# Optimization experiments

Hardware: AMD Instinct MI355X
Metric: run time of the kernel (lower is better)

Reference implementation:

```python
import jax, jax.numpy as jnp
import numpy as np

HID = 768          # args.hidden_size
LSTM2 = 768        # args.lstm_dim * 2
SCALE = HID ** -0.5


def _cross_attn(q_in, kv_in, Wq, bq, Wk, bk, Wv, bv):
    # Linear projections (weights stored as [in, out])
    Q = q_in @ Wq + bq            # [B, Sq, H]
    K = kv_in @ Wk + bk           # [B, Sk, H]
    V = kv_in @ Wv + bv           # [B, Sk, H]
    attn = jnp.einsum('bqh,bkh->bqk', Q, K) * SCALE
    attn = jax.nn.softmax(attn, axis=-1)
    return jnp.einsum('bqk,bkh->bqh', attn, V)


def setup_inputs() -> dict:
    key = jax.random.key(0)
    ks = jax.random.split(key, 14)
    B, Ssyn, Ssem = 4, 4096, 2048
    syntactic_feat = jax.random.normal(ks[0], (B, Ssyn, LSTM2), jnp.float32)
    semantic_feat = jax.random.normal(ks[1], (B, Ssem, HID), jnp.float32)

    def lin(k, fan_in, fan_out):
        kw, kb = jax.random.split(k)
        bound = 1.0 / np.sqrt(fan_in)
        W = jax.random.uniform(kw, (fan_in, fan_out), jnp.float32, -bound, bound)
        b = jax.random.uniform(kb, (fan_out,), jnp.float32, -bound, bound)
        return W, b

    # syntax_to_semantic: query_dim=HID, key_dim=LSTM2
    Wq1, bq1 = lin(ks[2], HID, HID)
    Wk1, bk1 = lin(ks[3], LSTM2, HID)
    Wv1, bv1 = lin(ks[4], LSTM2, HID)
    # semantic_to_syntax: query_dim=LSTM2, key_dim=HID
    Wq2, bq2 = lin(ks[5], LSTM2, HID)
    Wk2, bk2 = lin(ks[6], HID, HID)
    Wv2, bv2 = lin(ks[7], HID, HID)
    return dict(syntactic_feat=syntactic_feat, semantic_feat=semantic_feat,
                Wq1=Wq1, bq1=bq1, Wk1=Wk1, bk1=bk1, Wv1=Wv1, bv1=bv1,
                Wq2=Wq2, bq2=bq2, Wk2=Wk2, bk2=bk2, Wv2=Wv2, bv2=bv2)


def reference(syntactic_feat, semantic_feat,
              Wq1, bq1, Wk1, bk1, Wv1, bv1,
              Wq2, bq2, Wk2, bk2, Wv2, bv2):
    # enhanced_semantic: queries from semantic, keys/values from syntactic
    enhanced_semantic = _cross_attn(semantic_feat, syntactic_feat,
                                    Wq1, bq1, Wk1, bk1, Wv1, bv1)
    # enhanced_syntax: queries from syntactic, keys/values from semantic
    enhanced_syntax = _cross_attn(syntactic_feat, semantic_feat,
                                  Wq2, bq2, Wk2, bk2, Wv2, bv2)
    return enhanced_semantic, enhanced_syntax
```

## Files before the change

kernel.cpp:

```cpp
#include <hip/hip_runtime.h>
#include <stdint.h>


typedef unsigned short u16;
typedef __attribute__((ext_vector_type(8))) __bf16 bf16x8;
typedef __attribute__((ext_vector_type(4))) float f32x4;

__device__ __forceinline__ float bf2f(u16 u) {
  union { unsigned int i; float f; } x; x.i = ((unsigned int)u) << 16; return x.f;
}
__device__ __forceinline__ u16 f2bf(float f) {
  union { float f; unsigned int i; } x; x.f = f;
  unsigned int i = x.i;
  i += 0x7fffu + ((i >> 16) & 1u);
  return (u16)(i >> 16);
}

__device__ __forceinline__ void cp16(void* lds, const void* g) {
  __builtin_amdgcn_global_load_lds((__attribute__((address_space(1))) void*)g,
                                   (__attribute__((address_space(3))) void*)lds,
                                   16, 0, 0);
}

struct GemmDesc {
  const u16* A; const u16* Bt; const float* bias; void* C;
  long sA, sB, sC;
  int K, lda, ldb, ldc;
  int gx, gy;
  int start;
  int mode, outf;
  float scale;
};
struct GemmPack { GemmDesc d[6]; int nd; };

__global__ __launch_bounds__(256)
void gemm_multi_kernel(GemmPack p)
{
  __shared__ __align__(16) u16 Asl[128 * 32];
  __shared__ __align__(16) u16 Bsl[128 * 32];

  int seg = 0;
#pragma unroll
  for (int t = 1; t < 6; ++t)
    if (t < p.nd && (int)blockIdx.x >= p.d[t].start) seg = t;
  const GemmDesc& g = p.d[seg];
  const int local = (int)blockIdx.x - g.start;
  const int pxy = g.gx * g.gy;
  const int bz = local / pxy;
  const int rem = local - bz * pxy;
  const int by = rem / g.gx;
  const int bx = rem - by * g.gx;

  const int tid  = threadIdx.x;
  const int lane = tid & 63;
  const int wave = tid >> 6;
  const int l15  = lane & 15;
  const int quad = lane >> 4;
  const int mw   = (wave >> 1) * 64;
  const int nw   = (wave & 1) * 64;

  const char* Ab = (const char*)(g.A + (long)bz * g.sA + (long)bx * 128 * g.lda);
  const char* Bb = (const char*)(g.Bt + (long)bz * g.sB + (long)by * 128 * g.ldb);

  const int o   = wave * 1024 + lane * 16;
  const int mst = o >> 6;
  const int cl  = (o >> 4) & 3;
  const int sst = (mst + (mst >> 2)) & 3;
  const int off = (cl ^ sst) << 4;
  char* ldsA = (char*)Asl + wave * 1024;
  char* ldsB = (char*)Bsl + wave * 1024;
  const long ldaB = (long)g.lda * 2;
  const long ldbB = (long)g.ldb * 2;
  const char* pa0 = Ab + (long)mst * ldaB + off;
  const char* pb0 = Bb + (long)mst * ldbB + off;

  int ia[4], ib[4];
#pragma unroll
  for (int i = 0; i < 4; ++i) {
    const int m = mw + i * 16 + l15;
    ia[i] = m * 4 + (quad ^ ((m + (m >> 2)) & 3));
    const int n = nw + i * 16 + l15;
    ib[i] = n * 4 + (quad ^ ((n + (n >> 2)) & 3));
  }

  f32x4 acc[4][4];
  {
    f32x4 zz = {0.f, 0.f, 0.f, 0.f};
#pragma unroll
    for (int i = 0; i < 4; ++i)
#pragma unroll
      for (int j = 0; j < 4; ++j) acc[i][j] = zz;
  }

  const int nk = g.K >> 5;
  for (int kk = 0; kk < nk; ++kk) {
    const long kb = (long)kk << 6;
    cp16(ldsA,        pa0 + kb);
    cp16(ldsA + 4096, pa0 + kb + 64 * ldaB);
    cp16(ldsB,        pb0 + kb);
    cp16(ldsB + 4096, pb0 + kb + 64 * ldbB);
    __syncthreads();

    bf16x8 a[4], b[4];
    const bf16x8* As8 = (const bf16x8*)Asl;
    const bf16x8* Bs8 = (const bf16x8*)Bsl;
#pragma unroll
    for (int i = 0; i < 4; ++i) a[i] = As8[ia[i]];
#pragma unroll
    for (int j = 0; j < 4; ++j) b[j] = Bs8[ib[j]];
#pragma unroll
    for (int i = 0; i < 4; ++i)
#pragma unroll
      for (int j = 0; j < 4; ++j)
        acc[i][j] = __builtin_amdgcn_mfma_f32_16x16x32_bf16(a[i], b[j], acc[i][j], 0, 0, 0);
    __syncthreads();
  }

  const int brow = bx * 128 + mw + quad * 4;
  const int bcol = by * 128 + nw + l15;
  float cb[4];
  if (g.mode == 1) {
#pragma unroll
    for (int j = 0; j < 4; ++j) cb[j] = g.bias[bcol + j * 16];
  }
#pragma unroll
  for (int i = 0; i < 4; ++i) {
    const int r0 = brow + i * 16;
    float rb[4];
    if (g.mode == 2) {
#pragma unroll
      for (int r = 0; r < 4; ++r) rb[r] = g.bias[r0 + r];
    }
#pragma unroll
    for (int j = 0; j < 4; ++j) {
      const int col = bcol + j * 16;
#pragma unroll
      for (int r = 0; r < 4; ++r) {
        float x = acc[i][j][r] * g.scale;
        if (g.mode == 1) x += cb[j];
        if (g.mode == 2) x += rb[r];
        const long idx = (long)bz * g.sC + (long)(r0 + r) * g.ldc + col;
        if (g.outf) ((float*)g.C)[idx] = x;
        else        ((u16*)g.C)[idx] = f2bf(x);
      }
    }
  }
}

__global__ __launch_bounds__(256)
void cvt2_bf16_kernel(const float* __restrict__ sa, u16* __restrict__ da, int n8a,
                      const float* __restrict__ sb, u16* __restrict__ db, int n8b)
{
  int idx = blockIdx.x * 256 + threadIdx.x;
  const float* src; u16* dst; int i;
  if (idx < n8a) { src = sa; dst = da; i = idx; }
  else           { src = sb; dst = db; i = idx - n8a; if (i >= n8b) return; }
  const float4* s4 = (const float4*)src;
  float4 a = s4[i * 2], b = s4[i * 2 + 1];
  uint4 o;
  o.x = (unsigned int)f2bf(a.x) | ((unsigned int)f2bf(a.y) << 16);
  o.y = (unsigned int)f2bf(a.z) | ((unsigned int)f2bf(a.w) << 16);
  o.z = (unsigned int)f2bf(b.x) | ((unsigned int)f2bf(b.y) << 16);
  o.w = (unsigned int)f2bf(b.z) | ((unsigned int)f2bf(b.w) << 16);
  ((uint4*)dst)[i] = o;
}

__global__ void transpose6_kernel(const float* s0, const float* s1, const float* s2,
                                  const float* s3, const float* s4, const float* s5,
                                  u16* d0, u16* d1, u16* d2,
                                  u16* d3, u16* d4, u16* d5)
{
  __shared__ float t[32][33];
  const float* src; u16* dst;
  switch (blockIdx.z) {
    case 0: src = s0; dst = d0; break;
    case 1: src = s1; dst = d1; break;
    case 2: src = s2; dst = d2; break;
    case 3: src = s3; dst = d3; break;
    case 4: src = s4; dst = d4; break;
    default: src = s5; dst = d5; break;
  }
  const int tx = threadIdx.x, ty = threadIdx.y;
  const int x = blockIdx.x * 32 + tx;
  const int y0 = blockIdx.y * 32;
#pragma unroll
  for (int j = 0; j < 32; j += 8) t[ty + j][tx] = src[(long)(y0 + ty + j) * 768 + x];
  __syncthreads();
  const int x2 = y0 + tx;
#pragma unroll
  for (int j = 0; j < 32; j += 8)
    dst[(long)(blockIdx.x * 32 + ty + j) * 768 + x2] = f2bf(t[tx][ty + j]);
}

template <int NV>
__device__ __forceinline__ void softmax_row(u16* row)
{
  __shared__ float red[8];
  const int tid  = threadIdx.x;
  const int lane = tid & 63;
  const int wave = tid >> 6;
  uint4* p4 = (uint4*)row;

  uint4 ld[NV / 8];
#pragma unroll
  for (int c = 0; c < NV / 8; ++c) ld[c] = p4[tid + c * 256];
  float v[NV];
#pragma unroll
  for (int c = 0; c < NV / 8; ++c) {
    unsigned int w[4] = {ld[c].x, ld[c].y, ld[c].z, ld[c].w};
#pragma unroll
    for (int q = 0; q < 4; ++q) {
      v[c * 8 + q * 2]     = bf2f((u16)(w[q] & 0xffffu));
      v[c * 8 + q * 2 + 1] = bf2f((u16)(w[q] >> 16));
    }
  }

  float m = -1e30f;
#pragma unroll
  for (int i = 0; i < NV; ++i) m = fmaxf(m, v[i]);
#pragma unroll
  for (int off = 32; off > 0; off >>= 1) m = fmaxf(m, __shfl_xor(m, off, 64));
  if (lane == 0) red[wave] = m;
  __syncthreads();
  m = fmaxf(fmaxf(red[0], red[1]), fmaxf(red[2], red[3]));

  float s = 0.f;
#pragma unroll
  for (int i = 0; i < NV; ++i) { v[i] = __expf(v[i] - m); s += v[i]; }
#pragma unroll
  for (int off = 32; off > 0; off >>= 1) s += __shfl_xor(s, off, 64);
  if (lane == 0) red[4 + wave] = s;
  __syncthreads();
  s = (red[4] + red[5]) + (red[6] + red[7]);
  const float inv = 1.0f / s;

#pragma unroll
  for (int c = 0; c < NV / 8; ++c) {
    unsigned int w[4];
#pragma unroll
    for (int q = 0; q < 4; ++q) {
      const u16 lo = f2bf(v[c * 8 + q * 2] * inv);
      const u16 hi = f2bf(v[c * 8 + q * 2 + 1] * inv);
      w[q] = (unsigned int)lo | ((unsigned int)hi << 16);
    }
    uint4 st; st.x = w[0]; st.y = w[1]; st.z = w[2]; st.w = w[3];
    p4[tid + c * 256] = st;
  }
}

__global__ __launch_bounds__(256)
void softmax_both_kernel(u16* S1, u16* S2)
{
  if (blockIdx.x < 8192) softmax_row<16>(S1 + (long)blockIdx.x * 4096);
  else                   softmax_row<8>(S2 + (long)(blockIdx.x - 8192) * 2048);
}


static GemmDesc mkdesc(const void* A, const void* Bt, const float* bias, void* C,
                       long sA, long sB, long sC, int K, int lda, int ldb, int ldc,
                       int M, int N, int start, int mode, int outf, float scale)
{
  GemmDesc d;
  d.A = (const u16*)A; d.Bt = (const u16*)Bt; d.bias = bias; d.C = C;
  d.sA = sA; d.sB = sB; d.sC = sC;
  d.K = K; d.lda = lda; d.ldb = ldb; d.ldc = ldc;
  d.gx = M / 128; d.gy = N / 128; d.start = start;
  d.mode = mode; d.outf = outf; d.scale = scale;
  return d;
}

extern "C" void kernel_launch(void* const* d_in, const int* in_sizes, int n_in,
                              void* d_out, int out_size, void* d_ws, size_t ws_size,
                              hipStream_t stream)
{
  (void)in_sizes; (void)n_in; (void)out_size; (void)ws_size;
  const float* syn = (const float*)d_in[0];
  const float* sem = (const float*)d_in[1];
  const float* W[6]    = {(const float*)d_in[2], (const float*)d_in[4],  (const float*)d_in[6],
                          (const float*)d_in[8], (const float*)d_in[10], (const float*)d_in[12]};
  const float* bias[6] = {(const float*)d_in[3], (const float*)d_in[5],  (const float*)d_in[7],
                          (const float*)d_in[9], (const float*)d_in[11], (const float*)d_in[13]};
  float* out = (float*)d_out;

  u16* ws   = (u16*)d_ws;
  u16* S1   = ws;
  u16* synb = ws;
  u16* semb = ws + 12582912;
  u16* WT   = ws + 18874368;
  u16* S2   = ws + 33554432;
  u16* V1T  = ws + 67108864;
  u16* Q1   = ws + 79691776;
  u16* V2Tc = ws + 79691776;
  u16* K1  = (u16*)out;
  u16* o1  = (u16*)(out + 6291456);
  u16* Q2  = o1;
  u16* K2  = o1 + 12582912;
  u16* V2T = o1 + 18874368;

  const float SC = 0.036084391824351615f;

  cvt2_bf16_kernel<<<dim3(9216), dim3(256), 0, stream>>>(
      syn, synb, 1572864, sem, semb, 786432);

  transpose6_kernel<<<dim3(24, 24, 6), dim3(32, 8, 1), 0, stream>>>(
      W[0], W[1], W[2], W[3], W[4], W[5],
      WT + 0 * 589824, WT + 1 * 589824, WT + 2 * 589824,
      WT + 3 * 589824, WT + 4 * 589824, WT + 5 * 589824);

  {
    GemmPack p; p.nd = 6;
    p.d[0] = mkdesc(synb, WT + 1 * 589824, bias[1], K1, 0, 0, 0,
                    768, 768, 768, 768, 16384, 768, 0, 1, 0, 1.f);
    p.d[1] = mkdesc(synb, WT + 3 * 589824, bias[3], Q2, 0, 0, 0,
                    768, 768, 768, 768, 16384, 768, 768, 1, 0, 1.f);
    p.d[2] = mkdesc(WT + 2 * 589824, synb, bias[2], V1T, 0, 0, 0,
                    768, 768, 768, 16384, 768, 16384, 1536, 2, 0, 1.f);
    p.d[3] = mkdesc(semb, WT + 0 * 589824, bias[0], Q1, 0, 0, 0,
                    768, 768, 768, 768, 8192, 768, 2304, 1, 0, 1.f);
    p.d[4] = mkdesc(semb, WT + 4 * 589824, bias[4], K2, 0, 0, 0,
                    768, 768, 768, 768, 8192, 768, 2688, 1, 0, 1.f);
    p.d[5] = mkdesc(WT + 5 * 589824, semb, bias[5], V2T, 0, 0, 0,
                    768, 768, 768, 8192, 768, 8192, 3072, 2, 0, 1.f);
    gemm_multi_kernel<<<dim3(3456), dim3(256), 0, stream>>>(p);
  }

  {
    GemmPack p; p.nd = 2;
    p.d[0] = mkdesc(Q1, K1, nullptr, S1,
                    1572864L, 3145728L, 8388608L,
                    768, 768, 768, 4096, 2048, 4096, 0, 0, 0, SC);
    p.d[1] = mkdesc(Q2, K2, nullptr, S2,
                    3145728L, 1572864L, 8388608L,
                    768, 768, 768, 2048, 4096, 2048, 2048, 0, 0, SC);
    gemm_multi_kernel<<<dim3(4096), dim3(256), 0, stream>>>(p);
  }

  softmax_both_kernel<<<dim3(24576), dim3(256), 0, stream>>>(S1, S2);

  hipMemcpyAsync(V2Tc, V2T, 12582912, hipMemcpyDeviceToDevice, stream);

  {
    GemmPack p; p.nd = 2;
    p.d[0] = mkdesc(S1, V1T, nullptr, out,
                    8388608L, 4096L, 1572864L,
                    4096, 4096, 16384, 768, 2048, 768, 0, 0, 1, 1.f);
    p.d[1] = mkdesc(S2, V2Tc, nullptr, out + 6291456,
                    8388608L, 2048L, 3145728L,
                    2048, 2048, 8192, 768, 4096, 768, 384, 0, 1, 1.f);
    gemm_multi_kernel<<<dim3(1152), dim3(256), 0, stream>>>(p);
  }
}
```

Baseline: 633.7 us.

## Double GEMM K-tile to 64, vectorize epilogue stores, fuse copy into softmax

The GEMM now stages a 64-wide K slice per iteration (two MFMA sub-steps) with a new XOR swizzle, which halves the number of barrier pairs per tile. The MFMA operands are swapped so each lane owns four consecutive output columns. That allows float4 or packed bf16x4 stores and a float4 bias load in the epilogue instead of scalar stores. The device-to-device memcpy is folded into extra blocks of the softmax kernel to save a separate launch. LDS use doubles to 32KB per block, which may reduce occupancy.

```diff
diff --git a/kernel.cpp b/kernel.cpp
--- a/kernel.cpp
+++ b/kernel.cpp
@@ -36,8 +36,8 @@
 __global__ __launch_bounds__(256)
 void gemm_multi_kernel(GemmPack p)
 {
-  __shared__ __align__(16) u16 Asl[128 * 32];
-  __shared__ __align__(16) u16 Bsl[128 * 32];
+  __shared__ __align__(16) u16 Asl[128 * 64];
+  __shared__ __align__(16) u16 Bsl[128 * 64];
 
   int seg = 0;
 #pragma unroll
@@ -62,26 +62,25 @@
   const char* Ab = (const char*)(g.A + (long)bz * g.sA + (long)bx * 128 * g.lda);
   const char* Bb = (const char*)(g.Bt + (long)bz * g.sB + (long)by * 128 * g.ldb);
 
-  const int o   = wave * 1024 + lane * 16;
-  const int mst = o >> 6;
-  const int cl  = (o >> 4) & 3;
-  const int sst = (mst + (mst >> 2)) & 3;
-  const int off = (cl ^ sst) << 4;
+  const int srow  = wave * 8 + (lane >> 3);
+  const int gchk  = (lane & 7) ^ (lane >> 3);
+  const long ldaB = (long)g.lda * 2;
+  const long ldbB = (long)g.ldb * 2;
+  const char* pa00 = Ab + (long)srow * ldaB + (gchk << 4);
+  const char* pb00 = Bb + (long)srow * ldbB + (gchk << 4);
   char* ldsA = (char*)Asl + wave * 1024;
   char* ldsB = (char*)Bsl + wave * 1024;
-  const long ldaB = (long)g.lda * 2;
-  const long ldbB = (long)g.ldb * 2;
-  const char* pa0 = Ab + (long)mst * ldaB + off;
-  const char* pb0 = Bb + (long)mst * ldbB + off;
-
-  int ia[4], ib[4];
-#pragma unroll
-  for (int i = 0; i < 4; ++i) {
-    const int m = mw + i * 16 + l15;
-    ia[i] = m * 4 + (quad ^ ((m + (m >> 2)) & 3));
-    const int n = nw + i * 16 + l15;
-    ib[i] = n * 4 + (quad ^ ((n + (n >> 2)) & 3));
-  }
+
+  int ia[2][4], ib[2][4];
+#pragma unroll
+  for (int s = 0; s < 2; ++s)
+#pragma unroll
+    for (int i = 0; i < 4; ++i) {
+      const int m = mw + i * 16 + l15;
+      ia[s][i] = m * 8 + ((s * 4 + quad) ^ (l15 & 7));
+      const int n = nw + i * 16 + l15;
+      ib[s][i] = n * 8 + ((s * 4 + quad) ^ (l15 & 7));
+    }
 
   f32x4 acc[4][4];
   {
@@ -92,56 +91,61 @@
       for (int j = 0; j < 4; ++j) acc[i][j] = zz;
   }
 
-  const int nk = g.K >> 5;
+  const int nk = g.K >> 6;
   for (int kk = 0; kk < nk; ++kk) {
-    const long kb = (long)kk << 6;
-    cp16(ldsA,        pa0 + kb);
-    cp16(ldsA + 4096, pa0 + kb + 64 * ldaB);
-    cp16(ldsB,        pb0 + kb);
-    cp16(ldsB + 4096, pb0 + kb + 64 * ldbB);
+    const long kb = (long)kk << 7;
+#pragma unroll
+    for (int r = 0; r < 4; ++r) {
+      cp16(ldsA + r * 4096, pa00 + kb + (long)r * 32 * ldaB);
+      cp16(ldsB + r * 4096, pb00 + kb + (long)r * 32 * ldbB);
+    }
     __syncthreads();
 
-    bf16x8 a[4], b[4];
     const bf16x8* As8 = (const bf16x8*)Asl;
     const bf16x8* Bs8 = (const bf16x8*)Bsl;
 #pragma unroll
-    for (int i = 0; i < 4; ++i) a[i] = As8[ia[i]];
-#pragma unroll
-    for (int j = 0; j < 4; ++j) b[j] = Bs8[ib[j]];
-#pragma unroll
-    for (int i = 0; i < 4; ++i)
-#pragma unroll
-      for (int j = 0; j < 4; ++j)
-        acc[i][j] = __builtin_amdgcn_mfma_f32_16x16x32_bf16(a[i], b[j], acc[i][j], 0, 0, 0);
+    for (int s = 0; s < 2; ++s) {
+      bf16x8 a[4], b[4];
+#pragma unroll
+      for (int i = 0; i < 4; ++i) a[i] = As8[ia[s][i]];
+#pragma unroll
+      for (int j = 0; j < 4; ++j) b[j] = Bs8[ib[s][j]];
+#pragma unroll
+      for (int i = 0; i < 4; ++i)
+#pragma unroll
+        for (int j = 0; j < 4; ++j)
+          acc[i][j] = __builtin_amdgcn_mfma_f32_16x16x32_bf16(b[j], a[i], acc[i][j], 0, 0, 0);
+    }
     __syncthreads();
   }
 
-  const int brow = bx * 128 + mw + quad * 4;
-  const int bcol = by * 128 + nw + l15;
-  float cb[4];
-  if (g.mode == 1) {
-#pragma unroll
-    for (int j = 0; j < 4; ++j) cb[j] = g.bias[bcol + j * 16];
-  }
+  const long cbase = (long)bz * g.sC;
 #pragma unroll
   for (int i = 0; i < 4; ++i) {
-    const int r0 = brow + i * 16;
-    float rb[4];
-    if (g.mode == 2) {
-#pragma unroll
-      for (int r = 0; r < 4; ++r) rb[r] = g.bias[r0 + r];
-    }
+    const int row = bx * 128 + mw + i * 16 + l15;
+    const float rbias = (g.mode == 2) ? g.bias[row] : 0.f;
 #pragma unroll
     for (int j = 0; j < 4; ++j) {
-      const int col = bcol + j * 16;
-#pragma unroll
-      for (int r = 0; r < 4; ++r) {
-        float x = acc[i][j][r] * g.scale;
-        if (g.mode == 1) x += cb[j];
-        if (g.mode == 2) x += rb[r];
-        const long idx = (long)bz * g.sC + (long)(r0 + r) * g.ldc + col;
-        if (g.outf) ((float*)g.C)[idx] = x;
-        else        ((u16*)g.C)[idx] = f2bf(x);
+      const int colbase = by * 128 + nw + j * 16 + quad * 4;
+      float v[4];
+#pragma unroll
+      for (int r = 0; r < 4; ++r) v[r] = acc[i][j][r] * g.scale;
+      if (g.mode == 1) {
+        const float4 cb = *(const float4*)(g.bias + colbase);
+        v[0] += cb.x; v[1] += cb.y; v[2] += cb.z; v[3] += cb.w;
+      } else if (g.mode == 2) {
+#pragma unroll
+        for (int r = 0; r < 4; ++r) v[r] += rbias;
+      }
+      const long idx = cbase + (long)row * g.ldc + colbase;
+      if (g.outf) {
+        float4 st; st.x = v[0]; st.y = v[1]; st.z = v[2]; st.w = v[3];
+        *(float4*)((float*)g.C + idx) = st;
+      } else {
+        uint2 st;
+        st.x = (unsigned int)f2bf(v[0]) | ((unsigned int)f2bf(v[1]) << 16);
+        st.y = (unsigned int)f2bf(v[2]) | ((unsigned int)f2bf(v[3]) << 16);
+        *(uint2*)((u16*)g.C + idx) = st;
       }
     }
   }
@@ -249,10 +253,15 @@
 }
 
 __global__ __launch_bounds__(256)
-void softmax_both_kernel(u16* S1, u16* S2)
-{
-  if (blockIdx.x < 8192) softmax_row<16>(S1 + (long)blockIdx.x * 4096);
-  else                   softmax_row<8>(S2 + (long)(blockIdx.x - 8192) * 2048);
+void softmax_both_kernel(u16* S1, u16* S2, const u16* cpy_src, u16* cpy_dst)
+{
+  if (blockIdx.x < 8192) { softmax_row<16>(S1 + (long)blockIdx.x * 4096); return; }
+  if (blockIdx.x < 24576) { softmax_row<8>(S2 + (long)(blockIdx.x - 8192) * 2048); return; }
+  const long base = (long)(blockIdx.x - 24576) * 512 + threadIdx.x;
+  const uint4* s = (const uint4*)cpy_src;
+  uint4* d = (uint4*)cpy_dst;
+  d[base] = s[base];
+  d[base + 256] = s[base + 256];
 }
 
 
@@ -335,9 +344,7 @@
     gemm_multi_kernel<<<dim3(4096), dim3(256), 0, stream>>>(p);
   }
 
-  softmax_both_kernel<<<dim3(24576), dim3(256), 0, stream>>>(S1, S2);
-
-  hipMemcpyAsync(V2Tc, V2T, 12582912, hipMemcpyDeviceToDevice, stream);
+  softmax_both_kernel<<<dim3(26112), dim3(256), 0, stream>>>(S1, S2, V2T, V2Tc);
 
   {
     GemmPack p; p.nd = 2;
```

Measured after the change: 581.9 us. -8.2%, faster.
